# Performance work log

Hardware: AMD Instinct MI355X
Metric: run time of the kernel (lower is better)

Reference implementation:

```python
import jax, jax.numpy as jnp
import numpy as np

SEQ_LEN = 256
INPUT_DIM = 1
HIDDEN = 1024
CLASSES = 10
BATCH = 256


def _uniform_param(key, shape, fan):
    # matches torch _parameter: uniform(-1/sqrt(y), 1/sqrt(y)), y = shape[1] if rank>1 else 1
    stdv = 1.0 / np.sqrt(fan)
    return jax.random.uniform(key, shape, jnp.float32, -stdv, stdv)


def setup_inputs() -> dict:
    key = jax.random.key(0)
    k0, k1, k2, k3, k4, k5 = jax.random.split(key, 6)
    x = jax.random.normal(k0, (BATCH, SEQ_LEN), jnp.float32)
    return {
        "x": x,
        "W_hx": _uniform_param(k1, (INPUT_DIM, HIDDEN), HIDDEN),
        "W_hh": _uniform_param(k2, (HIDDEN, HIDDEN), HIDDEN),
        "W_ph": _uniform_param(k3, (HIDDEN, CLASSES), CLASSES),
        "b_h": _uniform_param(k4, (HIDDEN,), 1),
        "b_p": _uniform_param(k5, (CLASSES,), 1),
    }


def reference(x, W_hx, W_hh, W_ph, b_h, b_p):
    # With INPUT_DIM == 1, x[:, t:t+1] is just column t; build [seq, batch, 1] for scan.
    xs = jnp.swapaxes(x, 0, 1)[:, :, None]  # [S, B, 1]
    h0 = jnp.zeros((x.shape[0], HIDDEN), x.dtype)

    def step(h_prev, x_t):
        h_t = jnp.tanh(x_t @ W_hx + h_prev @ W_hh + b_h)  # [B, H]
        return h_t, None

    h_last, _ = jax.lax.scan(step, h0, xs)
    # Original computes p_t each step but only returns the last; compute only the last.
    return h_last @ W_ph + b_p  # [B, C]
```

## Files before the change

kernel.cpp:

```cpp
#include <hip/hip_runtime.h>
#include <stdint.h>

#define SEQ   256
#define BATCH 256
#define HID   1024
#define NCLS  10

#define NWG     128
#define THREADS 512
#define PLANEB  (32 * 16 * 64 * 16)

typedef __attribute__((ext_vector_type(8))) short bf16x8;
typedef __attribute__((ext_vector_type(4))) float f32x4;
typedef __attribute__((ext_vector_type(4))) unsigned int u32x4;

__device__ __forceinline__ unsigned short f2bf(float f) {
  unsigned u = __builtin_bit_cast(unsigned, f);
  u = (u + 0x7FFFu + ((u >> 16) & 1u)) >> 16;
  return (unsigned short)u;
}
__device__ __forceinline__ float bf2f(unsigned short h) {
  unsigned u = ((unsigned)h) << 16;
  return __builtin_bit_cast(float, u);
}
__device__ __forceinline__ float fast_tanh(float x) {
  float ax = __builtin_fabsf(x);
  float e = __expf(2.0f * ax);
  float t = 1.0f - 2.0f / (e + 1.0f);
  return __builtin_copysignf(t, x);
}
__device__ __forceinline__ unsigned tag_of(unsigned t) {
  return ((t >> 1) & 1u) ^ 1u;
}

__global__ __launch_bounds__(THREADS, 1) void rnn_onebar(
    const float* __restrict__ x, const float* __restrict__ Whx,
    const float* __restrict__ Whh, const float* __restrict__ Wph,
    const float* __restrict__ bh, const float* __restrict__ bp,
    float* __restrict__ out, unsigned char* __restrict__ ws)
{
  __shared__ f32x4 red[2][4][2][7][64];

  const int tid  = threadIdx.x;
  const int lane = tid & 63;
  const int wv   = tid >> 6;
  const int l15  = lane & 15;
  const int q    = lane >> 4;

  const int gb = blockIdx.x >> 4;
  const int s  = blockIdx.x & 15;

  unsigned char* p0 = ws;
  unsigned char* p1 = ws + PLANEB;

  bf16x8 whi[4][4], wlo[4][4];
#pragma unroll
  for (int i = 0; i < 4; ++i) {
    const int ks = wv * 4 + i;
#pragma unroll
    for (int rt = 0; rt < 4; ++rt) {
      const int n = s * 64 + rt * 16 + l15;
#pragma unroll
      for (int j = 0; j < 8; ++j) {
        int k = ks * 32 + 4 * q + (j & 3) + 16 * (j >> 2);
        float w = Whh[(size_t)k * HID + n];
        unsigned short hi = f2bf(w);
        whi[i][rt][j] = (short)hi;
        wlo[i][rt][j] = (short)f2bf(w - bf2f(hi));
      }
    }
  }

  const int u_o  = wv >> 1, bt_oo = wv & 1;
  const int b_own = gb * 32 + bt_oo * 16 + l15;
  const float* xrow = x + (size_t)b_own * SEQ;
  float4 whxA, whxB, bhA, bhB;
  whxA = *(const float4*)(Whx + s * 64 + (2 * u_o) * 16 + q * 4);
  whxB = *(const float4*)(Whx + s * 64 + (2 * u_o + 1) * 16 + q * 4);
  bhA  = *(const float4*)(bh  + s * 64 + (2 * u_o) * 16 + q * 4);
  bhB  = *(const float4*)(bh  + s * 64 + (2 * u_o + 1) * 16 + q * 4);
  const size_t soff = ((size_t)((s * 2 + u_o) * 16 + gb * 2 + bt_oo) * 64 + lane) * 16;
  volatile u32x4* st0 = (volatile u32x4*)(p0 + soff);
  volatile u32x4* st1 = (volatile u32x4*)(p1 + soff);

  const size_t oA0 = ((size_t)((wv * 4 + 0) * 16 + gb * 2) * 64 + lane) * 16;
  const size_t oA1 = ((size_t)((wv * 4 + 1) * 16 + gb * 2) * 64 + lane) * 16;
  const size_t oA2 = ((size_t)((wv * 4 + 2) * 16 + gb * 2) * 64 + lane) * 16;
  const size_t oA3 = ((size_t)((wv * 4 + 3) * 16 + gb * 2) * 64 + lane) * 16;

  for (int t = 0; t < SEQ; ++t) {
    const unsigned tauW = tag_of((unsigned)t);
    const int buf = t & 1;

    f32x4 acc[4][2];
#pragma unroll
    for (int rt = 0; rt < 4; ++rt)
#pragma unroll
      for (int bt = 0; bt < 2; ++bt) acc[rt][bt] = (f32x4){0.f, 0.f, 0.f, 0.f};

    if (t > 0) {
      const unsigned tauR = tag_of((unsigned)(t - 1));
      const unsigned char* rp = (t & 1) ? p0 : p1;
      const unsigned char* b0 = rp + oA0;
      const unsigned char* b1 = rp + oA1;
      const unsigned char* b2 = rp + oA2;
      const unsigned char* b3 = rp + oA3;
      u32x4 f0, f1, f2, f3, f4, f5, f6, f7;

      for (;;) {
        asm volatile(
          "global_load_dwordx4 %0, %8, off sc0 sc1\n\t"
          "global_load_dwordx4 %1, %8, off offset:1024 sc0 sc1\n\t"
          "global_load_dwordx4 %2, %9, off sc0 sc1\n\t"
          "global_load_dwordx4 %3, %9, off offset:1024 sc0 sc1\n\t"
          "global_load_dwordx4 %4, %10, off sc0 sc1\n\t"
          "global_load_dwordx4 %5, %10, off offset:1024 sc0 sc1\n\t"
          "global_load_dwordx4 %6, %11, off sc0 sc1\n\t"
          "global_load_dwordx4 %7, %11, off offset:1024 sc0 sc1\n\t"
          "s_waitcnt vmcnt(0)"
          : "=&v"(f0), "=&v"(f1), "=&v"(f2), "=&v"(f3),
            "=&v"(f4), "=&v"(f5), "=&v"(f6), "=&v"(f7)
          : "v"(b0), "v"(b1), "v"(b2), "v"(b3)
          : "memory");
        __builtin_amdgcn_sched_barrier(0);
        unsigned vb = ((f0[0] ^ tauR) | (f0[1] ^ tauR) | (f0[2] ^ tauR) | (f0[3] ^ tauR) |
                       (f1[0] ^ tauR) | (f1[1] ^ tauR) | (f1[2] ^ tauR) | (f1[3] ^ tauR) |
                       (f2[0] ^ tauR) | (f2[1] ^ tauR) | (f2[2] ^ tauR) | (f2[3] ^ tauR) |
                       (f3[0] ^ tauR) | (f3[1] ^ tauR) | (f3[2] ^ tauR) | (f3[3] ^ tauR) |
                       (f4[0] ^ tauR) | (f4[1] ^ tauR) | (f4[2] ^ tauR) | (f4[3] ^ tauR) |
                       (f5[0] ^ tauR) | (f5[1] ^ tauR) | (f5[2] ^ tauR) | (f5[3] ^ tauR) |
                       (f6[0] ^ tauR) | (f6[1] ^ tauR) | (f6[2] ^ tauR) | (f6[3] ^ tauR) |
                       (f7[0] ^ tauR) | (f7[1] ^ tauR) | (f7[2] ^ tauR) | (f7[3] ^ tauR)) & 1u;
        if (__all((int)(vb == 0))) break;
        __builtin_amdgcn_s_sleep(1);
      }

#define MSTEP(F, I, BT)                                                        \
      { bf16x8 a_ = __builtin_bit_cast(bf16x8, F);                             \
        acc[0][BT] = __builtin_amdgcn_mfma_f32_16x16x32_bf16(whi[I][0], a_, acc[0][BT], 0, 0, 0); \
        acc[0][BT] = __builtin_amdgcn_mfma_f32_16x16x32_bf16(wlo[I][0], a_, acc[0][BT], 0, 0, 0); \
        acc[1][BT] = __builtin_amdgcn_mfma_f32_16x16x32_bf16(whi[I][1], a_, acc[1][BT], 0, 0, 0); \
        acc[1][BT] = __builtin_amdgcn_mfma_f32_16x16x32_bf16(wlo[I][1], a_, acc[1][BT], 0, 0, 0); \
        acc[2][BT] = __builtin_amdgcn_mfma_f32_16x16x32_bf16(whi[I][2], a_, acc[2][BT], 0, 0, 0); \
        acc[2][BT] = __builtin_amdgcn_mfma_f32_16x16x32_bf16(wlo[I][2], a_, acc[2][BT], 0, 0, 0); \
        acc[3][BT] = __builtin_amdgcn_mfma_f32_16x16x32_bf16(whi[I][3], a_, acc[3][BT], 0, 0, 0); \
        acc[3][BT] = __builtin_amdgcn_mfma_f32_16x16x32_bf16(wlo[I][3], a_, acc[3][BT], 0, 0, 0); }
      MSTEP(f0, 0, 0) MSTEP(f1, 0, 1) MSTEP(f2, 1, 0) MSTEP(f3, 1, 1)
      MSTEP(f4, 2, 0) MSTEP(f5, 2, 1) MSTEP(f6, 3, 0) MSTEP(f7, 3, 1)
#undef MSTEP
    }

#pragma unroll
    for (int T = 0; T < 8; ++T) {
      const int rt = T >> 1, bt = T & 1;
      const int o = (rt & 2) | bt;
      if (o != wv) {
        const int slot = (wv > o) ? (wv - 1) : wv;
        red[buf][rt][bt][slot][lane] = acc[rt][bt];
      }
    }
    __syncthreads();

    if (wv < 4) {
      f32x4 sA = acc[2 * u_o][bt_oo];
      f32x4 sB = acc[2 * u_o + 1][bt_oo];
#pragma unroll
      for (int pr = 0; pr < 7; ++pr) {
        sA += red[buf][2 * u_o][bt_oo][pr][lane];
        sB += red[buf][2 * u_o + 1][bt_oo][pr][lane];
      }
      const float xb = xrow[t];
      const float a0 = fast_tanh(sA[0] + xb * whxA.x + bhA.x);
      const float a1 = fast_tanh(sA[1] + xb * whxA.y + bhA.y);
      const float a2 = fast_tanh(sA[2] + xb * whxA.z + bhA.z);
      const float a3 = fast_tanh(sA[3] + xb * whxA.w + bhA.w);
      const float c0 = fast_tanh(sB[0] + xb * whxB.x + bhB.x);
      const float c1 = fast_tanh(sB[1] + xb * whxB.y + bhB.y);
      const float c2 = fast_tanh(sB[2] + xb * whxB.z + bhB.z);
      const float c3 = fast_tanh(sB[3] + xb * whxB.w + bhB.w);
      u32x4 stv;
      stv[0] = (((unsigned)f2bf(a0) | ((unsigned)f2bf(a1) << 16)) & ~1u) | tauW;
      stv[1] = (((unsigned)f2bf(a2) | ((unsigned)f2bf(a3) << 16)) & ~1u) | tauW;
      stv[2] = (((unsigned)f2bf(c0) | ((unsigned)f2bf(c1) << 16)) & ~1u) | tauW;
      stv[3] = (((unsigned)f2bf(c2) | ((unsigned)f2bf(c3) << 16)) & ~1u) | tauW;
      if (t & 1) *st1 = stv; else *st0 = stv;
    }
  }

  if (s != 0) return;
  {
    const unsigned tauF = tag_of(255u);
    u32x4 hf[4][2];
    for (;;) {
#pragma unroll
      for (int i = 0; i < 4; ++i)
#pragma unroll
        for (int bt = 0; bt < 2; ++bt)
          hf[i][bt] = *(const volatile u32x4*)
              (p1 + ((size_t)((wv * 4 + i) * 16 + gb * 2 + bt) * 64 + lane) * 16);
      unsigned bad = 0;
#pragma unroll
      for (int i = 0; i < 4; ++i)
#pragma unroll
        for (int bt = 0; bt < 2; ++bt)
#pragma unroll
          for (int w = 0; w < 4; ++w) bad |= (hf[i][bt][w] ^ tauF) & 1u;
      if (__all((int)(bad == 0))) break;
      __builtin_amdgcn_s_sleep(2);
    }

    float pr0[NCLS], pr1[NCLS];
#pragma unroll
    for (int c = 0; c < NCLS; ++c) { pr0[c] = 0.f; pr1[c] = 0.f; }
#pragma unroll
    for (int i = 0; i < 4; ++i) {
      const int ks = wv * 4 + i;
#pragma unroll
      for (int bt = 0; bt < 2; ++bt) {
#pragma unroll
        for (int w = 0; w < 4; ++w) {
          unsigned word = hf[i][bt][w];
#pragma unroll
          for (int h2 = 0; h2 < 2; ++h2) {
            int j = 2 * w + h2;
            int k = ks * 32 + 4 * q + (j & 3) + 16 * (j >> 2);
            float hv = bf2f((unsigned short)(h2 ? (word >> 16) : (word & 0xffffu)));
            const float* wrow = Wph + (size_t)k * NCLS;
#pragma unroll
            for (int c = 0; c < NCLS; ++c) {
              if (bt == 0) pr0[c] += hv * wrow[c];
              else         pr1[c] += hv * wrow[c];
            }
          }
        }
      }
    }
#pragma unroll
    for (int c = 0; c < NCLS; ++c) {
      pr0[c] += __shfl_xor(pr0[c], 16, 64); pr0[c] += __shfl_xor(pr0[c], 32, 64);
      pr1[c] += __shfl_xor(pr1[c], 16, 64); pr1[c] += __shfl_xor(pr1[c], 32, 64);
    }
    float* projl = (float*)&red[0][0][0][0][0];
    if (q == 0) {
#pragma unroll
      for (int c = 0; c < NCLS; ++c) {
        projl[((wv * 2 + 0) * 16 + l15) * NCLS + c] = pr0[c];
        projl[((wv * 2 + 1) * 16 + l15) * NCLS + c] = pr1[c];
      }
    }
    __syncthreads();
    if (tid < 32 * NCLS) {
      int bl = tid / NCLS, c = tid - bl * NCLS;
      float sum = bp[c];
#pragma unroll
      for (int w = 0; w < 8; ++w)
        sum += projl[((w * 2 + (bl >> 4)) * 16 + (bl & 15)) * NCLS + c];
      out[(size_t)(gb * 32 + bl) * NCLS + c] = sum;
    }
  }
}

extern "C" void kernel_launch(void* const* d_in, const int* in_sizes, int n_in,
                              void* d_out, int out_size, void* d_ws, size_t ws_size,
                              hipStream_t stream) {
  const float* x   = (const float*)d_in[0];
  const float* Whx = (const float*)d_in[1];
  const float* Whh = (const float*)d_in[2];
  const float* Wph = (const float*)d_in[3];
  const float* bh  = (const float*)d_in[4];
  const float* bp  = (const float*)d_in[5];

  hipLaunchKernelGGL(rnn_onebar, dim3(NWG), dim3(THREADS), 0, stream,
                     x, Whx, Whh, Wph, bh, bp,
                     (float*)d_out, (unsigned char*)d_ws);
}
```

Before: 1.273 ms.

## Prefetch next-step hidden state speculatively with double-buffered polling loads

Issues the loads for the next step's hidden state right after the LDS barrier, once before and once after the tanh/store phase. The first batch that carries the expected tag is used, so the cross-workgroup flag-poll latency overlaps the reduction and activation work. The input sequence is also staged in LDS at kernel start, which removes a global load per step. The cost is more in-flight loads and extra registers, plus hand-tuned vmcnt waits that depend on exact load counts.

Result: slower. 2.644 ms (+107.7%).

```diff
diff --git a/kernel.cpp b/kernel.cpp
--- a/kernel.cpp
+++ b/kernel.cpp
@@ -33,13 +33,49 @@
   return ((t >> 1) & 1u) ^ 1u;
 }
 
-__global__ __launch_bounds__(THREADS, 1) void rnn_onebar(
+#define ISSUE8(A0,A1,A2,A3,A4,A5,A6,A7, B0,B1,B2,B3)                           \
+  asm volatile(                                                                \
+    "global_load_dwordx4 %0, %8, off sc0 sc1\n\t"                              \
+    "global_load_dwordx4 %1, %8, off offset:1024 sc0 sc1\n\t"                  \
+    "global_load_dwordx4 %2, %9, off sc0 sc1\n\t"                              \
+    "global_load_dwordx4 %3, %9, off offset:1024 sc0 sc1\n\t"                  \
+    "global_load_dwordx4 %4, %10, off sc0 sc1\n\t"                             \
+    "global_load_dwordx4 %5, %10, off offset:1024 sc0 sc1\n\t"                 \
+    "global_load_dwordx4 %6, %11, off sc0 sc1\n\t"                             \
+    "global_load_dwordx4 %7, %11, off offset:1024 sc0 sc1"                     \
+    : "=&v"(A0),"=&v"(A1),"=&v"(A2),"=&v"(A3),                                 \
+      "=&v"(A4),"=&v"(A5),"=&v"(A6),"=&v"(A7)                                  \
+    : "v"(B0),"v"(B1),"v"(B2),"v"(B3)                                          \
+    : "memory")
+
+#define WAIT8() do { asm volatile("s_waitcnt vmcnt(8)" ::: "memory");          \
+                     __builtin_amdgcn_sched_barrier(0); } while (0)
+#define WAIT9() do { asm volatile("s_waitcnt vmcnt(9)" ::: "memory");          \
+                     __builtin_amdgcn_sched_barrier(0); } while (0)
+#define DRAIN() do { asm volatile("s_waitcnt vmcnt(0)" ::: "memory");          \
+                     __builtin_amdgcn_sched_barrier(0); } while (0)
+
+#define CHECK8(A0,A1,A2,A3,A4,A5,A6,A7, TAU) ({                                \
+  unsigned vb_ = ((A0[0]^TAU)|(A0[1]^TAU)|(A0[2]^TAU)|(A0[3]^TAU)|             \
+                  (A1[0]^TAU)|(A1[1]^TAU)|(A1[2]^TAU)|(A1[3]^TAU)|             \
+                  (A2[0]^TAU)|(A2[1]^TAU)|(A2[2]^TAU)|(A2[3]^TAU)|             \
+                  (A3[0]^TAU)|(A3[1]^TAU)|(A3[2]^TAU)|(A3[3]^TAU)|             \
+                  (A4[0]^TAU)|(A4[1]^TAU)|(A4[2]^TAU)|(A4[3]^TAU)|             \
+                  (A5[0]^TAU)|(A5[1]^TAU)|(A5[2]^TAU)|(A5[3]^TAU)|             \
+                  (A6[0]^TAU)|(A6[1]^TAU)|(A6[2]^TAU)|(A6[3]^TAU)|             \
+                  (A7[0]^TAU)|(A7[1]^TAU)|(A7[2]^TAU)|(A7[3]^TAU)) & 1u;       \
+  __all((int)(vb_ == 0)); })
+
+#define BARRIER() asm volatile("s_waitcnt lgkmcnt(0)\n\ts_barrier" ::: "memory")
+
+__global__ __launch_bounds__(THREADS, 1) void rnn_pipe(
     const float* __restrict__ x, const float* __restrict__ Whx,
     const float* __restrict__ Whh, const float* __restrict__ Wph,
     const float* __restrict__ bh, const float* __restrict__ bp,
     float* __restrict__ out, unsigned char* __restrict__ ws)
 {
   __shared__ f32x4 red[2][4][2][7][64];
+  __shared__ float x_lds[32][257];
 
   const int tid  = threadIdx.x;
   const int lane = tid & 63;
@@ -52,6 +88,11 @@
 
   unsigned char* p0 = ws;
   unsigned char* p1 = ws + PLANEB;
+
+  for (int idx = tid; idx < 32 * 256; idx += THREADS) {
+    int row = idx >> 8, tt = idx & 255;
+    x_lds[row][tt] = x[(size_t)(gb * 32 + row) * SEQ + tt];
+  }
 
   bf16x8 whi[4][4], wlo[4][4];
 #pragma unroll
@@ -72,14 +113,13 @@
   }
 
   const int u_o  = wv >> 1, bt_oo = wv & 1;
-  const int b_own = gb * 32 + bt_oo * 16 + l15;
-  const float* xrow = x + (size_t)b_own * SEQ;
+  const int u_c  = (wv < 4) ? u_o : 0;
   float4 whxA, whxB, bhA, bhB;
-  whxA = *(const float4*)(Whx + s * 64 + (2 * u_o) * 16 + q * 4);
-  whxB = *(const float4*)(Whx + s * 64 + (2 * u_o + 1) * 16 + q * 4);
-  bhA  = *(const float4*)(bh  + s * 64 + (2 * u_o) * 16 + q * 4);
-  bhB  = *(const float4*)(bh  + s * 64 + (2 * u_o + 1) * 16 + q * 4);
-  const size_t soff = ((size_t)((s * 2 + u_o) * 16 + gb * 2 + bt_oo) * 64 + lane) * 16;
+  whxA = *(const float4*)(Whx + s * 64 + (2 * u_c) * 16 + q * 4);
+  whxB = *(const float4*)(Whx + s * 64 + (2 * u_c + 1) * 16 + q * 4);
+  bhA  = *(const float4*)(bh  + s * 64 + (2 * u_c) * 16 + q * 4);
+  bhB  = *(const float4*)(bh  + s * 64 + (2 * u_c + 1) * 16 + q * 4);
+  const size_t soff = ((size_t)((s * 2 + u_c) * 16 + gb * 2 + bt_oo) * 64 + lane) * 16;
   volatile u32x4* st0 = (volatile u32x4*)(p0 + soff);
   volatile u32x4* st1 = (volatile u32x4*)(p1 + soff);
 
@@ -88,52 +128,7 @@
   const size_t oA2 = ((size_t)((wv * 4 + 2) * 16 + gb * 2) * 64 + lane) * 16;
   const size_t oA3 = ((size_t)((wv * 4 + 3) * 16 + gb * 2) * 64 + lane) * 16;
 
-  for (int t = 0; t < SEQ; ++t) {
-    const unsigned tauW = tag_of((unsigned)t);
-    const int buf = t & 1;
-
-    f32x4 acc[4][2];
-#pragma unroll
-    for (int rt = 0; rt < 4; ++rt)
-#pragma unroll
-      for (int bt = 0; bt < 2; ++bt) acc[rt][bt] = (f32x4){0.f, 0.f, 0.f, 0.f};
-
-    if (t > 0) {
-      const unsigned tauR = tag_of((unsigned)(t - 1));
-      const unsigned char* rp = (t & 1) ? p0 : p1;
-      const unsigned char* b0 = rp + oA0;
-      const unsigned char* b1 = rp + oA1;
-      const unsigned char* b2 = rp + oA2;
-      const unsigned char* b3 = rp + oA3;
-      u32x4 f0, f1, f2, f3, f4, f5, f6, f7;
-
-      for (;;) {
-        asm volatile(
-          "global_load_dwordx4 %0, %8, off sc0 sc1\n\t"
-          "global_load_dwordx4 %1, %8, off offset:1024 sc0 sc1\n\t"
-          "global_load_dwordx4 %2, %9, off sc0 sc1\n\t"
-          "global_load_dwordx4 %3, %9, off offset:1024 sc0 sc1\n\t"
-          "global_load_dwordx4 %4, %10, off sc0 sc1\n\t"
-          "global_load_dwordx4 %5, %10, off offset:1024 sc0 sc1\n\t"
-          "global_load_dwordx4 %6, %11, off sc0 sc1\n\t"
-          "global_load_dwordx4 %7, %11, off offset:1024 sc0 sc1\n\t"
-          "s_waitcnt vmcnt(0)"
-          : "=&v"(f0), "=&v"(f1), "=&v"(f2), "=&v"(f3),
-            "=&v"(f4), "=&v"(f5), "=&v"(f6), "=&v"(f7)
-          : "v"(b0), "v"(b1), "v"(b2), "v"(b3)
-          : "memory");
-        __builtin_amdgcn_sched_barrier(0);
-        unsigned vb = ((f0[0] ^ tauR) | (f0[1] ^ tauR) | (f0[2] ^ tauR) | (f0[3] ^ tauR) |
-                       (f1[0] ^ tauR) | (f1[1] ^ tauR) | (f1[2] ^ tauR) | (f1[3] ^ tauR) |
-                       (f2[0] ^ tauR) | (f2[1] ^ tauR) | (f2[2] ^ tauR) | (f2[3] ^ tauR) |
-                       (f3[0] ^ tauR) | (f3[1] ^ tauR) | (f3[2] ^ tauR) | (f3[3] ^ tauR) |
-                       (f4[0] ^ tauR) | (f4[1] ^ tauR) | (f4[2] ^ tauR) | (f4[3] ^ tauR) |
-                       (f5[0] ^ tauR) | (f5[1] ^ tauR) | (f5[2] ^ tauR) | (f5[3] ^ tauR) |
-                       (f6[0] ^ tauR) | (f6[1] ^ tauR) | (f6[2] ^ tauR) | (f6[3] ^ tauR) |
-                       (f7[0] ^ tauR) | (f7[1] ^ tauR) | (f7[2] ^ tauR) | (f7[3] ^ tauR)) & 1u;
-        if (__all((int)(vb == 0))) break;
-        __builtin_amdgcn_s_sleep(1);
-      }
+  __syncthreads();
 
 #define MSTEP(F, I, BT)                                                        \
       { bf16x8 a_ = __builtin_bit_cast(bf16x8, F);                             \
@@ -145,9 +140,44 @@
         acc[2][BT] = __builtin_amdgcn_mfma_f32_16x16x32_bf16(wlo[I][2], a_, acc[2][BT], 0, 0, 0); \
         acc[3][BT] = __builtin_amdgcn_mfma_f32_16x16x32_bf16(whi[I][3], a_, acc[3][BT], 0, 0, 0); \
         acc[3][BT] = __builtin_amdgcn_mfma_f32_16x16x32_bf16(wlo[I][3], a_, acc[3][BT], 0, 0, 0); }
-      MSTEP(f0, 0, 0) MSTEP(f1, 0, 1) MSTEP(f2, 1, 0) MSTEP(f3, 1, 1)
-      MSTEP(f4, 2, 0) MSTEP(f5, 2, 1) MSTEP(f6, 3, 0) MSTEP(f7, 3, 1)
-#undef MSTEP
+#define MBLOCK(F0,F1,F2,F3,F4,F5,F6,F7)                                        \
+      MSTEP(F0, 0, 0) MSTEP(F1, 0, 1) MSTEP(F2, 1, 0) MSTEP(F3, 1, 1)          \
+      MSTEP(F4, 2, 0) MSTEP(F5, 2, 1) MSTEP(F6, 3, 0) MSTEP(F7, 3, 1)
+
+  u32x4 P0, P1, P2, P3, P4, P5, P6, P7;
+  u32x4 Q0, Q1, Q2, Q3, Q4, Q5, Q6, Q7;
+  const unsigned char *b0 = p0, *b1 = p0, *b2 = p0, *b3 = p0;
+
+  for (int t = 0; t < SEQ; ++t) {
+    const unsigned tauW = tag_of((unsigned)t);
+    const int buf = t & 1;
+
+    f32x4 acc[4][2];
+#pragma unroll
+    for (int rt = 0; rt < 4; ++rt)
+#pragma unroll
+      for (int bt = 0; bt < 2; ++bt) acc[rt][bt] = (f32x4){0.f, 0.f, 0.f, 0.f};
+
+    if (t > 0) {
+      const unsigned tauR = tag_of((unsigned)(t - 1));
+      int useP;
+      if (wv < 4) WAIT9(); else WAIT8();
+      if (CHECK8(P0,P1,P2,P3,P4,P5,P6,P7, tauR)) {
+        useP = 1;
+      } else {
+        for (;;) {
+          ISSUE8(P0,P1,P2,P3,P4,P5,P6,P7, b0,b1,b2,b3);
+          WAIT8();
+          if (CHECK8(Q0,Q1,Q2,Q3,Q4,Q5,Q6,Q7, tauR)) { useP = 0; break; }
+          __builtin_amdgcn_s_sleep(1);
+          ISSUE8(Q0,Q1,Q2,Q3,Q4,Q5,Q6,Q7, b0,b1,b2,b3);
+          WAIT8();
+          if (CHECK8(P0,P1,P2,P3,P4,P5,P6,P7, tauR)) { useP = 1; break; }
+        }
+      }
+      DRAIN();
+      if (useP) { MBLOCK(P0,P1,P2,P3,P4,P5,P6,P7) }
+      else      { MBLOCK(Q0,Q1,Q2,Q3,Q4,Q5,Q6,Q7) }
     }
 
 #pragma unroll
@@ -159,17 +189,23 @@
         red[buf][rt][bt][slot][lane] = acc[rt][bt];
       }
     }
-    __syncthreads();
+    BARRIER();
+
+    const unsigned char* np = (t & 1) ? p1 : p0;
+    if (t + 1 < SEQ) {
+      b0 = np + oA0; b1 = np + oA1; b2 = np + oA2; b3 = np + oA3;
+      ISSUE8(P0,P1,P2,P3,P4,P5,P6,P7, b0,b1,b2,b3);
+    }
 
     if (wv < 4) {
-      f32x4 sA = acc[2 * u_o][bt_oo];
-      f32x4 sB = acc[2 * u_o + 1][bt_oo];
+      f32x4 sA = acc[2 * u_c][bt_oo];
+      f32x4 sB = acc[2 * u_c + 1][bt_oo];
 #pragma unroll
       for (int pr = 0; pr < 7; ++pr) {
-        sA += red[buf][2 * u_o][bt_oo][pr][lane];
-        sB += red[buf][2 * u_o + 1][bt_oo][pr][lane];
-      }
-      const float xb = xrow[t];
+        sA += red[buf][2 * u_c][bt_oo][pr][lane];
+        sB += red[buf][2 * u_c + 1][bt_oo][pr][lane];
+      }
+      const float xb = x_lds[bt_oo * 16 + l15][t];
       const float a0 = fast_tanh(sA[0] + xb * whxA.x + bhA.x);
       const float a1 = fast_tanh(sA[1] + xb * whxA.y + bhA.y);
       const float a2 = fast_tanh(sA[2] + xb * whxA.z + bhA.z);
@@ -185,6 +221,10 @@
       stv[3] = (((unsigned)f2bf(c2) | ((unsigned)f2bf(c3) << 16)) & ~1u) | tauW;
       if (t & 1) *st1 = stv; else *st0 = stv;
     }
+
+    if (t + 1 < SEQ) {
+      ISSUE8(Q0,Q1,Q2,Q3,Q4,Q5,Q6,Q7, b0,b1,b2,b3);
+    }
   }
 
   if (s != 0) return;
@@ -270,7 +310,7 @@
   const float* bh  = (const float*)d_in[4];
   const float* bp  = (const float*)d_in[5];
 
-  hipLaunchKernelGGL(rnn_onebar, dim3(NWG), dim3(THREADS), 0, stream,
+  hipLaunchKernelGGL(rnn_pipe, dim3(NWG), dim3(THREADS), 0, stream,
                      x, Whx, Whh, Wph, bh, bp,
                      (float*)d_out, (unsigned char*)d_ws);
 }
```
